# Optimization experiments

Measured on AMD Instinct MI355X. Metric: run time of the kernel, lower is better.

The kernel has to match this reference:

```python
import jax, jax.numpy as jnp
import numpy as np

TOP_K = 2
CAPACITY_FACTOR = 1.0


def setup_inputs() -> dict:
    key = jax.random.key(0)
    ks = jax.random.split(key, 4)
    S, M, E, V = 32768, 512, 64, 2048
    return {
        "x": jax.random.normal(ks[0], (S, M), jnp.float32),
        "wg": jax.random.normal(ks[1], (E, M), jnp.float32) * (1.0 / np.sqrt(M)),
        "fc1_w": jax.random.normal(ks[2], (E, M, V), jnp.float32) * (1.0 / np.sqrt(M)),
        "fc1_b": jnp.zeros((E, V), jnp.float32),
        "fc2_w": jax.random.normal(ks[3], (E, V, M), jnp.float32) * (1.0 / np.sqrt(V)),
        "fc2_b": jnp.zeros((E, M), jnp.float32),
    }


def _moe_forward(x, wg, fc1_w, fc1_b, fc2_w, fc2_b):
    S, M = x.shape
    E = wg.shape[0]
    K = TOP_K
    # capacity = top_k * int(cap_factor * ceil(S / E))  (static, from shapes)
    C = K * int(CAPACITY_FACTOR * ((S + E - 1) // E))

    # --- gating ---
    logits = x @ wg.T                                    # [S, E]
    gates = jax.nn.softmax(logits, axis=-1)              # [S, E]
    topk_idx = jax.lax.top_k(logits, K)[1]               # [S, K] int32
    masks = jax.nn.one_hot(topk_idx, E, dtype=logits.dtype)  # [S, K, E]
    gates_s = jnp.einsum('se,ske->sk', gates, masks)     # [S, K]

    # load-balance aux loss (fp32 path of load_balance)
    me = gates.sum(axis=0)                               # [E]
    ce = masks[:, 0, :].sum(axis=0)                      # [E]
    l_loss = jnp.sum(me * ce) * (E / (S * S))

    # --- cumsum capacity locations with per-k offsets (acc_base) ---
    counts = masks.sum(axis=0)                           # [K, E]
    prev_counts = jnp.concatenate(
        [jnp.zeros((1, E), logits.dtype), jnp.cumsum(counts, axis=0)[:-1]], axis=0)
    cums = jnp.cumsum(masks, axis=0) - 1.0               # fast_cumsum_sub_one per k
    locs = jnp.einsum('ske,ske->sk', cums + prev_counts[None], masks).astype(jnp.int32)

    # normalize top-k gates (top_k > 1 branch)
    denom = jnp.maximum(gates_s.sum(axis=1, keepdims=True),
                        jnp.finfo(gates_s.dtype).eps)
    gates_n = gates_s / denom                            # [S, K]

    # --- encode: scatter tokens into [E, C, M], overflow tokens dropped ---
    valid = locs < C                                     # [S, K]
    flat_pos = jnp.where(valid, topk_idx.astype(jnp.int32) * C + locs, E * C)
    src = jnp.broadcast_to(x[:, None, :], (S, K, M)).reshape(-1, M)
    disp = jnp.zeros((E * C + 1, M), x.dtype).at[flat_pos.reshape(-1)].add(src)
    disp = disp[:E * C].reshape(E, C, M)                 # world_size=1: AllToAll = id

    # --- fused FFN experts: relu(x @ fc1 + b1) @ fc2 + b2 ---
    h = jax.nn.relu(jnp.einsum('ecm,emv->ecv', disp, fc1_w) + fc1_b[:, None, :])
    eout = jnp.einsum('ecv,evm->ecm', h, fc2_w) + fc2_b[:, None, :]

    # --- decode/combine: gather expert slots, weight by normalized gates ---
    eflat = jnp.concatenate([eout.reshape(E * C, M),
                             jnp.zeros((1, M), eout.dtype)], axis=0)
    gathered = eflat[flat_pos]                           # [S, K, M]
    y = jnp.einsum('sk,skm->sm', gates_n * valid.astype(gates_n.dtype), gathered)
    return y, l_loss


def reference(x, wg, fc1_w, fc1_b, fc2_w, fc2_b):
    return _moe_forward(x, wg, fc1_w, fc1_b, fc2_w, fc2_b)
```

## Files before the change

### kernel.cpp

```cpp
#include <hip/hip_runtime.h>
#include <hip/hip_bf16.h>
#include <stdint.h>

#define S_TOK 32768
#define M_DIM 512
#define E_NUM 64
#define V_DIM 2048
#define CAP   1024

typedef __attribute__((ext_vector_type(8))) short short8;
typedef __attribute__((ext_vector_type(4))) float f32x4;

__device__ __forceinline__ unsigned short f2bf(float f) {
  unsigned int u = __float_as_uint(f);
  unsigned int r = (u + 0x7fffu + ((u >> 16) & 1u)) >> 16;
  return (unsigned short)r;
}
__device__ __forceinline__ float bf2f(unsigned short h) {
  return __uint_as_float(((unsigned int)h) << 16);
}

__device__ __forceinline__ void gload16(const void* g, void* lds) {
  __builtin_amdgcn_global_load_lds(
      (const __attribute__((address_space(1))) void*)g,
      (__attribute__((address_space(3))) void*)lds, 16, 0, 0);
}

__global__ __launch_bounds__(256) void transpose_convert(const float* __restrict__ in,
                                                         unsigned short* __restrict__ out,
                                                         int R, int Cc) {
  __shared__ float ts[64][65];
  int b = blockIdx.z;
  const float* ip = in + (size_t)b * R * Cc;
  unsigned short* op = out + (size_t)b * R * Cc;
  int c0 = blockIdx.x * 64, r0 = blockIdx.y * 64;
  int tid = threadIdx.x;
  int lrow = tid >> 4;
  int lc4 = (tid & 15) * 4;
  #pragma unroll
  for (int i = 0; i < 4; ++i) {
    int row = i * 16 + lrow;
    float4 v = *reinterpret_cast<const float4*>(&ip[(size_t)(r0 + row) * Cc + c0 + lc4]);
    ts[row][lc4 + 0] = v.x; ts[row][lc4 + 1] = v.y;
    ts[row][lc4 + 2] = v.z; ts[row][lc4 + 3] = v.w;
  }
  __syncthreads();
  #pragma unroll
  for (int i = 0; i < 2; ++i) {
    int chunk = i * 256 + tid;
    int c = chunk >> 3;
    int rg = (chunk & 7) * 8;
    short8 o;
    #pragma unroll
    for (int j = 0; j < 8; ++j) o[j] = (short)f2bf(ts[rg + j][c]);
    *reinterpret_cast<short8*>(&op[(size_t)(c0 + c) * R + r0 + rg]) = o;
  }
}

__global__ __launch_bounds__(256) void gating_kernel(
    const float* __restrict__ x, const float* __restrict__ wg,
    int* __restrict__ topk, float* __restrict__ gates_n,
    float* __restrict__ me_part, int* __restrict__ ce_part,
    unsigned short* __restrict__ xbf) {
  __shared__ float4 xs4[16 * 128];
  __shared__ float mered[4][64];
  __shared__ int cered[4][64];
  int tid = threadIdx.x;
  int l = tid & 63, w = tid >> 6;
  int tb = blockIdx.x * 16;
  const float4* xg4 = reinterpret_cast<const float4*>(x) + (size_t)tb * 128;
  ushort4* xb4 = reinterpret_cast<ushort4*>(xbf) + (size_t)tb * 128;
  #pragma unroll
  for (int i = 0; i < 8; ++i) {
    float4 v = xg4[i * 256 + tid];
    xs4[i * 256 + tid] = v;
    ushort4 o;
    o.x = f2bf(v.x); o.y = f2bf(v.y); o.z = f2bf(v.z); o.w = f2bf(v.w);
    xb4[i * 256 + tid] = o;
  }
  __syncthreads();

  const float4* wg4 = reinterpret_cast<const float4*>(wg) + (size_t)l * 128;
  float acc[4] = {0.f, 0.f, 0.f, 0.f};
  for (int i = 0; i < 128; ++i) {
    float4 wv = wg4[i];
    #pragma unroll
    for (int t = 0; t < 4; ++t) {
      float4 xv = xs4[(w * 4 + t) * 128 + i];
      acc[t] += xv.x * wv.x; acc[t] += xv.y * wv.y;
      acc[t] += xv.z * wv.z; acc[t] += xv.w * wv.w;
    }
  }

  float melocal = 0.f;
  int celocal = 0;
  for (int t = 0; t < 4; ++t) {
    float v = acc[t];
    float bv = v; int bi = l;
    #pragma unroll
    for (int off = 32; off; off >>= 1) {
      float ov = __shfl_xor(bv, off);
      int oi = __shfl_xor(bi, off);
      if (ov > bv || (ov == bv && oi < bi)) { bv = ov; bi = oi; }
    }
    float v2 = (l == bi) ? -INFINITY : v;
    float bv2 = v2; int bi2 = l;
    #pragma unroll
    for (int off = 32; off; off >>= 1) {
      float ov = __shfl_xor(bv2, off);
      int oi = __shfl_xor(bi2, off);
      if (ov > bv2 || (ov == bv2 && oi < bi2)) { bv2 = ov; bi2 = oi; }
    }
    float ex = expf(v - bv);
    float s = ex;
    #pragma unroll
    for (int off = 32; off; off >>= 1) s += __shfl_xor(s, off);
    melocal += ex / s;
    if (l == bi) celocal += 1;
    if (l == 0) {
      int sidx = tb + w * 4 + t;
      topk[sidx * 2 + 0] = bi;
      topk[sidx * 2 + 1] = bi2;
      float g1 = 1.0f / s;
      float g2 = expf(bv2 - bv) / s;
      float denom = fmaxf(g1 + g2, 1.1920929e-07f);
      gates_n[sidx * 2 + 0] = g1 / denom;
      gates_n[sidx * 2 + 1] = g2 / denom;
    }
  }
  mered[w][l] = melocal;
  cered[w][l] = celocal;
  __syncthreads();
  if (tid < 64) {
    me_part[blockIdx.x * 64 + tid] =
        mered[0][tid] + mered[1][tid] + mered[2][tid] + mered[3][tid];
    ce_part[blockIdx.x * 64 + tid] =
        cered[0][tid] + cered[1][tid] + cered[2][tid] + cered[3][tid];
  }
}

__global__ __launch_bounds__(256) void rank_kernel(const int* __restrict__ topk,
                                                   int* __restrict__ dest,
                                                   int* __restrict__ slot_map) {
  int e = blockIdx.x;
  int tid = threadIdx.x;
  int l = tid & 63, w = tid >> 6;
  const int2* tk = reinterpret_cast<const int2*>(topk);
  int base = tid * 128;
  int c0 = 0, c1 = 0;
  for (int j = 0; j < 128; ++j) {
    int2 p = tk[base + j];
    c0 += (p.x == e); c1 += (p.y == e);
  }
  int i0 = c0, i1 = c1;
  #pragma unroll
  for (int off = 1; off < 64; off <<= 1) {
    int t0 = __shfl_up(i0, off);
    int t1 = __shfl_up(i1, off);
    if (l >= off) { i0 += t0; i1 += t1; }
  }
  __shared__ int ws0[4], ws1[4], wo0[4], wo1[4], tot0s;
  if (l == 63) { ws0[w] = i0; ws1[w] = i1; }
  __syncthreads();
  if (tid == 0) {
    int a = 0, b = 0;
    #pragma unroll
    for (int j = 0; j < 4; ++j) { wo0[j] = a; a += ws0[j]; wo1[j] = b; b += ws1[j]; }
    tot0s = a;
  }
  __syncthreads();
  int loc0 = wo0[w] + i0 - c0;
  int loc1 = tot0s + wo1[w] + i1 - c1;
  for (int j = 0; j < 128; ++j) {
    int s = base + j;
    int2 p = tk[s];
    if (p.x == e) {
      int d = (loc0 < CAP) ? e * CAP + loc0 : -1;
      dest[s * 2] = d;
      if (d >= 0) slot_map[d] = s;
      loc0++;
    }
    if (p.y == e) {
      int d = (loc1 < CAP) ? e * CAP + loc1 : -1;
      dest[s * 2 + 1] = d;
      if (d >= 0) slot_map[d] = s;
      loc1++;
    }
  }
}

#define PH_TOP                                                                 \
  __builtin_amdgcn_sched_barrier(0);                                           \
  __builtin_amdgcn_s_barrier();                                                \
  asm volatile("s_waitcnt lgkmcnt(0)" ::: "memory");                           \
  __builtin_amdgcn_sched_barrier(0);                                           \
  __builtin_amdgcn_s_setprio(1);
#define PH_BOT                                                                 \
  __builtin_amdgcn_s_setprio(0);                                               \
  __builtin_amdgcn_sched_barrier(0);                                           \
  __builtin_amdgcn_s_barrier();

struct SmemGemm {
  union {
    struct {
      unsigned short A[2][256 * 64];
      unsigned short B[2][256 * 64];
    } st;
    unsigned short C[256 * 258];
  };
};

template <int KD, int ND, int NBX, int NBY, int NLOOP, bool GATHER, bool RELU>
__global__ __launch_bounds__(512, 2) void gemm8_kernel(
    const unsigned short* __restrict__ A,
    const unsigned short* __restrict__ BT,
    const float* __restrict__ bias,
    const int* __restrict__ slot_map,
    unsigned short* __restrict__ out) {
  constexpr int NT = KD / 64;
  constexpr int NBYG = NBY / NLOOP;
  __shared__ SmemGemm sm;

  const int tid = threadIdx.x;
  const int l = tid & 63;
  const int w = tid >> 6;
  const int wm = w >> 2;
  const int wn = w & 3;
  const int lr = l & 15;
  const int lk8 = l >> 4;

  const int nwg = E_NUM * NBX * NBYG;
  const int cpx = nwg >> 3;
  int lid = ((int)blockIdx.x % 8) * cpx + (int)blockIdx.x / 8;
  const int e = lid / (NBX * NBYG);
  int rem = lid % (NBX * NBYG);
  const int n0 = (rem / NBYG) * 256;
  const int r0base = (rem % NBYG) * (NLOOP * 256);

  const int cg8 = (((l & 7) ^ (l >> 3)) * 8);

  int arows[2][2];
  uint32_t offB[2][2], ldsA[2][2], ldsB[2][2];
  #pragma unroll
  for (int sel = 0; sel < 2; ++sel) {
    #pragma unroll
    for (int i = 0; i < 2; ++i) {
      int lr128 = i * 64 + w * 8 + (l >> 3);
      int ar = ((lr128 >> 6) * 128) + sel * 64 + (lr128 & 63);
      int br = ((lr128 >> 5) * 64) + sel * 32 + (lr128 & 31);
      arows[sel][i] = ar;
      ldsA[sel][i] = ar * 64 + (l & 7) * 8;
      ldsB[sel][i] = br * 64 + (l & 7) * 8;
      offB[sel][i] = (uint32_t)(n0 + br) * KD + cg8;
    }
  }
  const unsigned short* Bexp = BT + (size_t)e * ND * KD;

  const int sg0 = ((0 + lk8) ^ (lr & 7)) * 8;
  const int sg1 = ((4 + lk8) ^ (lr & 7)) * 8;

#define STAGE_A(sel, p, kt)                                                    \
  do {                                                                         \
    gload16(A + offA[sel][0] + (kt) * 64, &sm.st.A[p][ldsA[sel][0]]);          \
    gload16(A + offA[sel][1] + (kt) * 64, &sm.st.A[p][ldsA[sel][1]]);          \
  } while (0)
#define STAGE_B(sel, p, kt)                                                    \
  do {                                                                         \
    gload16(Bexp + offB[sel][0] + (kt) * 64, &sm.st.B[p][ldsB[sel][0]]);       \
    gload16(Bexp + offB[sel][1] + (kt) * 64, &sm.st.B[p][ldsB[sel][1]]);       \
  } while (0)
#define RD_A(p, mh, mi, ks)                                                    \
  (*reinterpret_cast<const short8*>(                                           \
      &sm.st.A[p][(wm * 128 + (mh) * 64 + (mi) * 16 + lr) * 64 + ((ks) ? sg1 : sg0)]))
#define RD_B(p, nh, ni, ks)                                                    \
  (*reinterpret_cast<const short8*>(                                           \
      &sm.st.B[p][(wn * 64 + (nh) * 32 + (ni) * 16 + lr) * 64 + ((ks) ? sg1 : sg0)]))

  short8 afr[2][4][2];
  short8 bfr[2][2];
  f32x4 acc[8][4];
  f32x4 zero = {0.f, 0.f, 0.f, 0.f};

  for (int it = 0; it < NLOOP; ++it) {
    const int r0 = r0base + it * 256;
    uint32_t offA[2][2];
    #pragma unroll
    for (int sel = 0; sel < 2; ++sel) {
      #pragma unroll
      for (int i = 0; i < 2; ++i) {
        int ar = arows[sel][i];
        int arow;
        if (GATHER) {
          int s = slot_map[e * CAP + r0 + ar];
          if (s < 0) s = 0;
          arow = s;
        } else {
          arow = e * CAP + r0 + ar;
        }
        offA[sel][i] = (uint32_t)arow * KD + cg8;
      }
    }
    #pragma unroll
    for (int m = 0; m < 8; ++m)
      #pragma unroll
      for (int n = 0; n < 4; ++n) acc[m][n] = zero;

    STAGE_A(0, 0, 0); STAGE_A(1, 0, 0); STAGE_B(0, 0, 0); STAGE_B(1, 0, 0);
    STAGE_A(0, 1, 1); STAGE_A(1, 1, 1); STAGE_B(0, 1, 1);
    asm volatile("s_waitcnt vmcnt(6)" ::: "memory");
    __builtin_amdgcn_sched_barrier(0);
    __builtin_amdgcn_s_barrier();

#define GROUP(k, p)                                                            \
  {                                                                            \
               \
    _Pragma("unroll") for (int mi = 0; mi < 4; ++mi) {                         \
      afr[0][mi][0] = RD_A(p, 0, mi, 0);                                       \
      afr[0][mi][1] = RD_A(p, 0, mi, 1);                                       \
    }                                                                          \
    _Pragma("unroll") for (int ni = 0; ni < 2; ++ni) {                         \
      bfr[ni][0] = RD_B(p, 0, ni, 0);                                          \
      bfr[ni][1] = RD_B(p, 0, ni, 1);                                          \
    }                                                                          \
    if ((k) + 1 < NT) { STAGE_B(1, (p) ^ 1, (k) + 1); }                        \
    PH_TOP                                                                     \
    _Pragma("unroll") for (int mi = 0; mi < 4; ++mi)                           \
      _Pragma("unroll") for (int ni = 0; ni < 2; ++ni) {                       \
        acc[mi][ni] = __builtin_amdgcn_mfma_f32_16x16x32_bf16(                 \
            afr[0][mi][0], bfr[ni][0], acc[mi][ni], 0, 0, 0);                  \
        acc[mi][ni] = __builtin_amdgcn_mfma_f32_16x16x32_bf16(                 \
            afr[0][mi][1], bfr[ni][1], acc[mi][ni], 0, 0, 0);                  \
      }                                                                        \
    PH_BOT                                                                     \
                 \
    _Pragma("unroll") for (int mi = 0; mi < 4; ++mi) {                         \
      afr[1][mi][0] = RD_A(p, 1, mi, 0);                                       \
      afr[1][mi][1] = RD_A(p, 1, mi, 1);                                       \
    }                                                                          \
    if ((k) + 2 < NT) { STAGE_A(0, p, (k) + 2); }                              \
    PH_TOP                                                                     \
    _Pragma("unroll") for (int mi = 0; mi < 4; ++mi)                           \
      _Pragma("unroll") for (int ni = 0; ni < 2; ++ni) {                       \
        acc[4 + mi][ni] = __builtin_amdgcn_mfma_f32_16x16x32_bf16(             \
            afr[1][mi][0], bfr[ni][0], acc[4 + mi][ni], 0, 0, 0);              \
        acc[4 + mi][ni] = __builtin_amdgcn_mfma_f32_16x16x32_bf16(             \
            afr[1][mi][1], bfr[ni][1], acc[4 + mi][ni], 0, 0, 0);              \
      }                                                                        \
    PH_BOT                                                                     \
                 \
    _Pragma("unroll") for (int ni = 0; ni < 2; ++ni) {                         \
      bfr[ni][0] = RD_B(p, 1, ni, 0);                                          \
      bfr[ni][1] = RD_B(p, 1, ni, 1);                                          \
    }                                                                          \
    if ((k) + 2 < NT) { STAGE_A(1, p, (k) + 2); }                              \
    PH_TOP                                                                     \
    _Pragma("unroll") for (int mi = 0; mi < 4; ++mi)                           \
      _Pragma("unroll") for (int ni = 0; ni < 2; ++ni) {                       \
        acc[mi][2 + ni] = __builtin_amdgcn_mfma_f32_16x16x32_bf16(             \
            afr[0][mi][0], bfr[ni][0], acc[mi][2 + ni], 0, 0, 0);              \
        acc[mi][2 + ni] = __builtin_amdgcn_mfma_f32_16x16x32_bf16(             \
            afr[0][mi][1], bfr[ni][1], acc[mi][2 + ni], 0, 0, 0);              \
      }                                                                        \
    PH_BOT                                                                     \
             \
    if ((k) + 2 < NT) { STAGE_B(0, p, (k) + 2); }                              \
    __builtin_amdgcn_sched_barrier(0);                                         \
    __builtin_amdgcn_s_barrier();                                              \
    __builtin_amdgcn_s_setprio(1);                                             \
    _Pragma("unroll") for (int mi = 0; mi < 4; ++mi)                           \
      _Pragma("unroll") for (int ni = 0; ni < 2; ++ni) {                       \
        acc[4 + mi][2 + ni] = __builtin_amdgcn_mfma_f32_16x16x32_bf16(         \
            afr[1][mi][0], bfr[ni][0], acc[4 + mi][2 + ni], 0, 0, 0);          \
        acc[4 + mi][2 + ni] = __builtin_amdgcn_mfma_f32_16x16x32_bf16(         \
            afr[1][mi][1], bfr[ni][1], acc[4 + mi][2 + ni], 0, 0, 0);          \
      }                                                                        \
    __builtin_amdgcn_s_setprio(0);                                             \
    __builtin_amdgcn_sched_barrier(0);                                         \
    if ((k) + 2 < NT) {                                                        \
      asm volatile("s_waitcnt vmcnt(6)" ::: "memory");                         \
    } else {                                                                   \
      asm volatile("s_waitcnt vmcnt(0)" ::: "memory");                         \
    }                                                                          \
    __builtin_amdgcn_sched_barrier(0);                                         \
    __builtin_amdgcn_s_barrier();                                              \
  }

    for (int kk = 0; kk < NT / 2; ++kk) {
      int k0 = 2 * kk;
      GROUP(k0, 0)
      GROUP(k0 + 1, 1)
    }
#undef GROUP

    #pragma unroll
    for (int n = 0; n < 4; ++n) {
      int gcl = wn * 64 + n * 16 + lr;
      float bv = bias[e * ND + n0 + gcl];
      #pragma unroll
      for (int m = 0; m < 8; ++m) {
        int trow = wm * 128 + m * 16 + lk8 * 4;
        #pragma unroll
        for (int j = 0; j < 4; ++j) {
          float v = acc[m][n][j] + bv;
          if (RELU) v = fmaxf(v, 0.f);
          sm.C[(trow + j) * 258 + gcl] = f2bf(v);
        }
      }
    }
    __syncthreads();
    #pragma unroll
    for (int i = 0; i < 16; ++i) {
      int chunk = i * 512 + tid;
      int row = chunk >> 5;
      int c8 = chunk & 31;
      short8 v = *reinterpret_cast<const short8*>(&sm.C[row * 258 + c8 * 8]);
      *reinterpret_cast<short8*>(
          &out[((size_t)(e * CAP + r0 + row)) * ND + n0 + c8 * 8]) = v;
    }
    asm volatile("s_waitcnt vmcnt(0)" ::: "memory");
    __syncthreads();
  }
#undef STAGE_A
#undef STAGE_B
#undef RD_A
#undef RD_B
}

__global__ __launch_bounds__(256) void decode_kernel(
    const unsigned short* __restrict__ Y, const int* __restrict__ dest,
    const float* __restrict__ gn, float* __restrict__ y) {
  int t = blockIdx.x * 4 + (threadIdx.x >> 6);
  int m0 = (threadIdx.x & 63) * 8;
  int d0 = dest[t * 2 + 0], d1 = dest[t * 2 + 1];
  float g0 = gn[t * 2 + 0], g1 = gn[t * 2 + 1];
  float o[8];
  #pragma unroll
  for (int j = 0; j < 8; ++j) o[j] = 0.f;
  if (d0 >= 0) {
    short8 v = *reinterpret_cast<const short8*>(&Y[(size_t)d0 * M_DIM + m0]);
    #pragma unroll
    for (int j = 0; j < 8; ++j) o[j] += g0 * bf2f((unsigned short)v[j]);
  }
  if (d1 >= 0) {
    short8 v = *reinterpret_cast<const short8*>(&Y[(size_t)d1 * M_DIM + m0]);
    #pragma unroll
    for (int j = 0; j < 8; ++j) o[j] += g1 * bf2f((unsigned short)v[j]);
  }
  float4 o0 = {o[0], o[1], o[2], o[3]};
  float4 o1 = {o[4], o[5], o[6], o[7]};
  *reinterpret_cast<float4*>(&y[(size_t)t * M_DIM + m0]) = o0;
  *reinterpret_cast<float4*>(&y[(size_t)t * M_DIM + m0 + 4]) = o1;
}

__global__ __launch_bounds__(1024) void loss_kernel(const float* __restrict__ me_part,
                                                    const int* __restrict__ ce_part,
                                                    float* __restrict__ out) {
  int tid = threadIdx.x;
  int e = tid & 63, ch = tid >> 6;
  float sme = 0.f, sce = 0.f;
  for (int j = 0; j < 128; ++j) {
    int idx = (ch * 128 + j) * 64 + e;
    sme += me_part[idx];
    sce += (float)ce_part[idx];
  }
  __shared__ float redm[16][64];
  __shared__ float redc[16][64];
  redm[ch][e] = sme;
  redc[ch][e] = sce;
  __syncthreads();
  if (tid < 64) {
    float m = 0.f, c = 0.f;
    #pragma unroll
    for (int k = 0; k < 16; ++k) { m += redm[k][tid]; c += redc[k][tid]; }
    float p = m * c;
    #pragma unroll
    for (int off = 32; off; off >>= 1) p += __shfl_xor(p, off);
    if (tid == 0) out[0] = p * ((float)E_NUM / ((float)S_TOK * (float)S_TOK));
  }
}

extern "C" void kernel_launch(void* const* d_in, const int* in_sizes, int n_in,
                              void* d_out, int out_size, void* d_ws, size_t ws_size,
                              hipStream_t stream) {
  const float* x     = (const float*)d_in[0];
  const float* wg    = (const float*)d_in[1];
  const float* fc1_w = (const float*)d_in[2];
  const float* fc1_b = (const float*)d_in[3];
  const float* fc2_w = (const float*)d_in[4];
  const float* fc2_b = (const float*)d_in[5];
  float* y = (float*)d_out;
  float* loss_out = y + (size_t)S_TOK * M_DIM;

  char* ws = (char*)d_ws;
  size_t off = 0;
  auto alloc = [&](size_t bytes) {
    char* p = ws + off;
    off += (bytes + 255) & ~(size_t)255;
    return p;
  };
  unsigned short* wT1 = (unsigned short*)alloc((size_t)E_NUM * V_DIM * M_DIM * 2);
  unsigned short* wT2 = (unsigned short*)alloc((size_t)E_NUM * M_DIM * V_DIM * 2);
  unsigned short* H   = (unsigned short*)alloc((size_t)E_NUM * CAP * V_DIM * 2);
  unsigned short* xbf = (unsigned short*)alloc((size_t)S_TOK * M_DIM * 2);
  int*   topk     = (int*)alloc((size_t)S_TOK * 2 * 4);
  float* gatesn   = (float*)alloc((size_t)S_TOK * 2 * 4);
  int*   dest     = (int*)alloc((size_t)S_TOK * 2 * 4);
  int*   slot_map = (int*)alloc((size_t)E_NUM * CAP * 4);
  float* me_part  = (float*)alloc((size_t)(S_TOK / 16) * 64 * 4);
  int*   ce_part  = (int*)alloc((size_t)(S_TOK / 16) * 64 * 4);
  unsigned short* Y = wT1;

  (void)hipMemsetAsync(slot_map, 0xFF, (size_t)E_NUM * CAP * 4, stream);

  transpose_convert<<<dim3(V_DIM / 64, M_DIM / 64, E_NUM), 256, 0, stream>>>(fc1_w, wT1, M_DIM, V_DIM);
  transpose_convert<<<dim3(M_DIM / 64, V_DIM / 64, E_NUM), 256, 0, stream>>>(fc2_w, wT2, V_DIM, M_DIM);

  gating_kernel<<<S_TOK / 16, 256, 0, stream>>>(x, wg, topk, gatesn, me_part, ce_part, xbf);
  rank_kernel<<<E_NUM, 256, 0, stream>>>(topk, dest, slot_map);

  gemm8_kernel<512, 2048, 8, 4, 4, true, true>
      <<<E_NUM * 8, 512, 0, stream>>>(xbf, wT1, fc1_b, slot_map, H);
  gemm8_kernel<2048, 512, 2, 4, 1, false, false>
      <<<E_NUM * 2 * 4, 512, 0, stream>>>(H, wT2, fc2_b, slot_map, Y);

  decode_kernel<<<S_TOK / 4, 256, 0, stream>>>(Y, dest, gatesn, y);
  loss_kernel<<<1, 1024, 0, stream>>>(me_part, ce_part, loss_out);
}
```

Before: 830.5 us.

## Loop over N tiles in FC1 GEMM, merge transposes, fold memset and loss kernels

The FC1 GEMM now keeps a fixed 256-row A tile (gathered token rows, loaded once) and loops over N tiles, where before it kept B fixed and looped over rows. The grid changes from 512 to 512 workgroups with a different row/column split. The two weight transpose launches become one launch, the slot_map memset moves into rank_kernel, and the loss reduction folds into an extra block of decode_kernel. This cuts launch overhead and changes which operand is reused across the loop, at the cost of a different L2 reuse pattern and a single-block loss tail inside decode.

```diff
diff --git a/kernel.cpp b/kernel.cpp
--- a/kernel.cpp
+++ b/kernel.cpp
@@ -26,14 +26,20 @@
       (__attribute__((address_space(3))) void*)lds, 16, 0, 0);
 }
 
-__global__ __launch_bounds__(256) void transpose_convert(const float* __restrict__ in,
-                                                         unsigned short* __restrict__ out,
-                                                         int R, int Cc) {
+__global__ __launch_bounds__(256) void transpose_convert2(const float* __restrict__ w1,
+                                                          unsigned short* __restrict__ o1,
+                                                          const float* __restrict__ w2,
+                                                          unsigned short* __restrict__ o2) {
   __shared__ float ts[64][65];
-  int b = blockIdx.z;
-  const float* ip = in + (size_t)b * R * Cc;
-  unsigned short* op = out + (size_t)b * R * Cc;
-  int c0 = blockIdx.x * 64, r0 = blockIdx.y * 64;
+  int which = blockIdx.z;
+  int R = which ? V_DIM : M_DIM;
+  int Cc = which ? M_DIM : V_DIM;
+  int nbx = Cc / 64;
+  int b = blockIdx.y;
+  const float* ip = (which ? w2 : w1) + (size_t)b * R * Cc;
+  unsigned short* op = (which ? o2 : o1) + (size_t)b * R * Cc;
+  int t = blockIdx.x;
+  int c0 = (t % nbx) * 64, r0 = (t / nbx) * 64;
   int tid = threadIdx.x;
   int lrow = tid >> 4;
   int lc4 = (tid & 15) * 4;
@@ -145,6 +151,9 @@
   int e = blockIdx.x;
   int tid = threadIdx.x;
   int l = tid & 63, w = tid >> 6;
+  int4 minus1 = {-1, -1, -1, -1};
+  reinterpret_cast<int4*>(slot_map + e * CAP)[tid] = minus1;
+
   const int2* tk = reinterpret_cast<const int2*>(topk);
   int base = tid * 128;
   int c0 = 0, c1 = 0;
@@ -210,7 +219,7 @@
   };
 };
 
-template <int KD, int ND, int NBX, int NBY, int NLOOP, bool GATHER, bool RELU>
+template <int KD, int ND, int NBX, int NBY, int NLOOPN, bool GATHER, bool RELU>
 __global__ __launch_bounds__(512, 2) void gemm8_kernel(
     const unsigned short* __restrict__ A,
     const unsigned short* __restrict__ BT,
@@ -218,7 +227,7 @@
     const int* __restrict__ slot_map,
     unsigned short* __restrict__ out) {
   constexpr int NT = KD / 64;
-  constexpr int NBYG = NBY / NLOOP;
+  constexpr int NBXG = NBX / NLOOPN;
   __shared__ SmemGemm sm;
 
   const int tid = threadIdx.x;
@@ -229,18 +238,18 @@
   const int lr = l & 15;
   const int lk8 = l >> 4;
 
-  const int nwg = E_NUM * NBX * NBYG;
+  const int nwg = E_NUM * NBXG * NBY;
   const int cpx = nwg >> 3;
   int lid = ((int)blockIdx.x % 8) * cpx + (int)blockIdx.x / 8;
-  const int e = lid / (NBX * NBYG);
-  int rem = lid % (NBX * NBYG);
-  const int n0 = (rem / NBYG) * 256;
-  const int r0base = (rem % NBYG) * (NLOOP * 256);
+  const int e = lid / (NBXG * NBY);
+  int rem = lid % (NBXG * NBY);
+  const int n0base = (rem / NBY) * (NLOOPN * 256);
+  const int r0 = (rem % NBY) * 256;
 
   const int cg8 = (((l & 7) ^ (l >> 3)) * 8);
 
-  int arows[2][2];
-  uint32_t offB[2][2], ldsA[2][2], ldsB[2][2];
+  int arows[2][2], brows[2][2];
+  uint32_t offA[2][2], ldsA[2][2], ldsB[2][2];
   #pragma unroll
   for (int sel = 0; sel < 2; ++sel) {
     #pragma unroll
@@ -249,9 +258,18 @@
       int ar = ((lr128 >> 6) * 128) + sel * 64 + (lr128 & 63);
       int br = ((lr128 >> 5) * 64) + sel * 32 + (lr128 & 31);
       arows[sel][i] = ar;
+      brows[sel][i] = br;
       ldsA[sel][i] = ar * 64 + (l & 7) * 8;
       ldsB[sel][i] = br * 64 + (l & 7) * 8;
-      offB[sel][i] = (uint32_t)(n0 + br) * KD + cg8;
+      int arow;
+      if (GATHER) {
+        int s = slot_map[e * CAP + r0 + ar];
+        if (s < 0) s = 0;
+        arow = s;
+      } else {
+        arow = e * CAP + r0 + ar;
+      }
+      offA[sel][i] = (uint32_t)arow * KD + cg8;
     }
   }
   const unsigned short* Bexp = BT + (size_t)e * ND * KD;
@@ -281,25 +299,15 @@
   f32x4 acc[8][4];
   f32x4 zero = {0.f, 0.f, 0.f, 0.f};
 
-  for (int it = 0; it < NLOOP; ++it) {
-    const int r0 = r0base + it * 256;
-    uint32_t offA[2][2];
-    #pragma unroll
-    for (int sel = 0; sel < 2; ++sel) {
+  for (int it = 0; it < NLOOPN; ++it) {
+    const int n0 = n0base + it * 256;
+    uint32_t offB[2][2];
+    #pragma unroll
+    for (int sel = 0; sel < 2; ++sel)
       #pragma unroll
-      for (int i = 0; i < 2; ++i) {
-        int ar = arows[sel][i];
-        int arow;
-        if (GATHER) {
-          int s = slot_map[e * CAP + r0 + ar];
-          if (s < 0) s = 0;
-          arow = s;
-        } else {
-          arow = e * CAP + r0 + ar;
-        }
-        offA[sel][i] = (uint32_t)arow * KD + cg8;
-      }
-    }
+      for (int i = 0; i < 2; ++i)
+        offB[sel][i] = (uint32_t)(n0 + brows[sel][i]) * KD + cg8;
+
     #pragma unroll
     for (int m = 0; m < 8; ++m)
       #pragma unroll
@@ -417,8 +425,10 @@
       *reinterpret_cast<short8*>(
           &out[((size_t)(e * CAP + r0 + row)) * ND + n0 + c8 * 8]) = v;
     }
-    asm volatile("s_waitcnt vmcnt(0)" ::: "memory");
-    __syncthreads();
+    if (it + 1 < NLOOPN) {
+      asm volatile("s_waitcnt vmcnt(0)" ::: "memory");
+      __syncthreads();
+    }
   }
 #undef STAGE_A
 #undef STAGE_B
@@ -428,9 +438,35 @@
 
 __global__ __launch_bounds__(256) void decode_kernel(
     const unsigned short* __restrict__ Y, const int* __restrict__ dest,
-    const float* __restrict__ gn, float* __restrict__ y) {
-  int t = blockIdx.x * 4 + (threadIdx.x >> 6);
-  int m0 = (threadIdx.x & 63) * 8;
+    const float* __restrict__ gn, float* __restrict__ y,
+    const float* __restrict__ me_part, const int* __restrict__ ce_part,
+    float* __restrict__ loss_out) {
+  int tid = threadIdx.x;
+  if (blockIdx.x == gridDim.x - 1) {
+    int e = tid & 63, ch = tid >> 6;
+    float sme = 0.f, sce = 0.f;
+    for (int j = 0; j < 512; ++j) {
+      int idx = (ch * 512 + j) * 64 + e;
+      sme += me_part[idx];
+      sce += (float)ce_part[idx];
+    }
+    __shared__ float redm[4][64];
+    __shared__ float redc[4][64];
+    redm[ch][e] = sme;
+    redc[ch][e] = sce;
+    __syncthreads();
+    if (tid < 64) {
+      float m = redm[0][tid] + redm[1][tid] + redm[2][tid] + redm[3][tid];
+      float c = redc[0][tid] + redc[1][tid] + redc[2][tid] + redc[3][tid];
+      float p = m * c;
+      #pragma unroll
+      for (int off = 32; off; off >>= 1) p += __shfl_xor(p, off);
+      if (tid == 0) loss_out[0] = p * ((float)E_NUM / ((float)S_TOK * (float)S_TOK));
+    }
+    return;
+  }
+  int t = blockIdx.x * 4 + (tid >> 6);
+  int m0 = (tid & 63) * 8;
   int d0 = dest[t * 2 + 0], d1 = dest[t * 2 + 1];
   float g0 = gn[t * 2 + 0], g1 = gn[t * 2 + 1];
   float o[8];
@@ -450,33 +486,6 @@
   float4 o1 = {o[4], o[5], o[6], o[7]};
   *reinterpret_cast<float4*>(&y[(size_t)t * M_DIM + m0]) = o0;
   *reinterpret_cast<float4*>(&y[(size_t)t * M_DIM + m0 + 4]) = o1;
-}
-
-__global__ __launch_bounds__(1024) void loss_kernel(const float* __restrict__ me_part,
-                                                    const int* __restrict__ ce_part,
-                                                    float* __restrict__ out) {
-  int tid = threadIdx.x;
-  int e = tid & 63, ch = tid >> 6;
-  float sme = 0.f, sce = 0.f;
-  for (int j = 0; j < 128; ++j) {
-    int idx = (ch * 128 + j) * 64 + e;
-    sme += me_part[idx];
-    sce += (float)ce_part[idx];
-  }
-  __shared__ float redm[16][64];
-  __shared__ float redc[16][64];
-  redm[ch][e] = sme;
-  redc[ch][e] = sce;
-  __syncthreads();
-  if (tid < 64) {
-    float m = 0.f, c = 0.f;
-    #pragma unroll
-    for (int k = 0; k < 16; ++k) { m += redm[k][tid]; c += redc[k][tid]; }
-    float p = m * c;
-    #pragma unroll
-    for (int off = 32; off; off >>= 1) p += __shfl_xor(p, off);
-    if (tid == 0) out[0] = p * ((float)E_NUM / ((float)S_TOK * (float)S_TOK));
-  }
 }
 
 extern "C" void kernel_launch(void* const* d_in, const int* in_sizes, int n_in,
@@ -510,19 +519,16 @@
   int*   ce_part  = (int*)alloc((size_t)(S_TOK / 16) * 64 * 4);
   unsigned short* Y = wT1;
 
-  (void)hipMemsetAsync(slot_map, 0xFF, (size_t)E_NUM * CAP * 4, stream);
-
-  transpose_convert<<<dim3(V_DIM / 64, M_DIM / 64, E_NUM), 256, 0, stream>>>(fc1_w, wT1, M_DIM, V_DIM);
-  transpose_convert<<<dim3(M_DIM / 64, V_DIM / 64, E_NUM), 256, 0, stream>>>(fc2_w, wT2, V_DIM, M_DIM);
+  transpose_convert2<<<dim3(256, E_NUM, 2), 256, 0, stream>>>(fc1_w, wT1, fc2_w, wT2);
 
   gating_kernel<<<S_TOK / 16, 256, 0, stream>>>(x, wg, topk, gatesn, me_part, ce_part, xbf);
   rank_kernel<<<E_NUM, 256, 0, stream>>>(topk, dest, slot_map);
 
   gemm8_kernel<512, 2048, 8, 4, 4, true, true>
-      <<<E_NUM * 8, 512, 0, stream>>>(xbf, wT1, fc1_b, slot_map, H);
+      <<<E_NUM * 2 * 4, 512, 0, stream>>>(xbf, wT1, fc1_b, slot_map, H);
   gemm8_kernel<2048, 512, 2, 4, 1, false, false>
       <<<E_NUM * 2 * 4, 512, 0, stream>>>(H, wT2, fc2_b, slot_map, Y);
 
-  decode_kernel<<<S_TOK / 4, 256, 0, stream>>>(Y, dest, gatesn, y);
-  loss_kernel<<<1, 1024, 0, stream>>>(me_part, ce_part, loss_out);
-}
+  decode_kernel<<<S_TOK / 4 + 1, 256, 0, stream>>>(Y, dest, gatesn, y,
+                                                   me_part, ce_part, loss_out);
+}
```

Result: slower. 873.4 us (+5.2%).
